# Performance work log

Measured on AMD Instinct MI355X. Metric: run time of the kernel, lower is better.

Reference implementation:

```python
import jax, jax.numpy as jnp
import numpy as np

# OGB feature vocab sizes
ATOM_DIMS = [119, 4, 12, 12, 10, 6, 6, 2, 2]
BOND_DIMS = [5, 6, 2]
ATOM_OFF = np.concatenate([[0], np.cumsum(ATOM_DIMS)[:-1]]).astype(np.int32)
BOND_OFF = np.concatenate([[0], np.cumsum(BOND_DIMS)[:-1]]).astype(np.int32)
SCHEDULE_LEN = 5   # len(train_schedule) == len(eval_schedule)
NUM_GRAPHS = 12000
BN_EPS = 1e-5

N_NODES, N_EDGES, HIDDEN, NUM_TASKS = 300000, 600000, 128, 128


def setup_inputs() -> dict:
    key = jax.random.key(0)
    ks = jax.random.split(key, 16)
    x = jax.random.randint(ks[0], (N_NODES, 9), 0, 2, dtype=jnp.int32)
    edge_index = jax.random.randint(ks[1], (2, N_EDGES), 0, N_NODES, dtype=jnp.int32)
    edge_attr = jax.random.randint(ks[2], (N_EDGES, 3), 0, 2, dtype=jnp.int32)
    batch = jnp.sort(jax.random.randint(ks[3], (N_NODES,), 0, NUM_GRAPHS, dtype=jnp.int32))
    # learned parameters (embedding tables concatenated with offsets)
    atom_emb = jax.random.normal(ks[4], (sum(ATOM_DIMS), HIDDEN), jnp.float32) * 0.1
    bond_emb = jax.random.normal(ks[5], (sum(BOND_DIMS), HIDDEN), jnp.float32) * 0.1
    conv_W = jax.random.normal(ks[6], (HIDDEN, HIDDEN), jnp.float32) * (1.0 / np.sqrt(HIDDEN))
    conv_b = jnp.zeros((HIDDEN,), jnp.float32)
    root_emb = jax.random.normal(ks[7], (HIDDEN,), jnp.float32) * 0.1
    bn_gamma = jnp.ones((HIDDEN,), jnp.float32)
    bn_beta = jnp.zeros((HIDDEN,), jnp.float32)
    bn_mean = jnp.zeros((HIDDEN,), jnp.float32)   # running stats (eval mode)
    bn_var = jnp.ones((HIDDEN,), jnp.float32)
    lin_W = jax.random.normal(ks[8], (NUM_TASKS, HIDDEN), jnp.float32) * (1.0 / np.sqrt(HIDDEN))
    lin_b = jnp.zeros((NUM_TASKS,), jnp.float32)
    return {"x": x, "edge_index": edge_index, "edge_attr": edge_attr, "batch": batch,
            "atom_emb": atom_emb, "bond_emb": bond_emb, "conv_W": conv_W, "conv_b": conv_b,
            "root_emb": root_emb, "bn_gamma": bn_gamma, "bn_beta": bn_beta,
            "bn_mean": bn_mean, "bn_var": bn_var, "lin_W": lin_W, "lin_b": lin_b}


def reference(x, edge_index, edge_attr, batch, atom_emb, bond_emb, conv_W, conv_b,
              root_emb, bn_gamma, bn_beta, bn_mean, bn_var, lin_W, lin_b):
    N = x.shape[0]
    # AtomEncoder / BondEncoder: sum of per-feature embedding lookups
    h = atom_emb[x + jnp.asarray(ATOM_OFF, x.dtype)].sum(axis=1)            # [N, H]
    e = bond_emb[edge_attr + jnp.asarray(BOND_OFF, edge_attr.dtype)].sum(axis=1)  # [E, H]
    row, col = edge_index[0], edge_index[1]
    deg = jax.ops.segment_sum(jnp.ones_like(row, h.dtype), row, num_segments=N) + 1.0  # [N]
    dis = deg ** -0.5                                                        # deg >= 1, no inf
    norm = dis[row] * dis[col]                                               # [E]
    inv_std = bn_gamma / jnp.sqrt(bn_var + BN_EPS)
    for i in range(SCHEDULE_LEN):
        old = h
        z = h @ conv_W.T + conv_b                                            # [N, H]
        # message: norm * relu(x_j + edge_emb), aggregated at target (col) via scatter-add
        msg = norm[:, None] * jax.nn.relu(z[row] + e)                        # [E, H]
        agg = jax.ops.segment_sum(msg, col, num_segments=N)                  # [N, H]
        z = agg + jax.nn.relu(z + root_emb) / deg[:, None]                   # self-loop term
        z = jax.nn.relu(z)
        z = (z - bn_mean) * inv_std + bn_beta                                # BN (eval, running stats)
        # dropout: identity in eval mode
        # NOTE: faithful to source bug: smooth_fac is the loop index i, not schedule[i]
        h = i * old + (1 - i) * z
    # global mean pool over graphs
    counts = jax.ops.segment_sum(jnp.ones((N,), h.dtype), batch, num_segments=NUM_GRAPHS)
    pooled = jax.ops.segment_sum(h, batch, num_segments=NUM_GRAPHS) / jnp.maximum(counts, 1.0)[:, None]
    return pooled @ lin_W.T + lin_b                                          # [num_graphs, num_tasks]
```

## Files before the change

### kernel.cpp

```cpp
#include <hip/hip_runtime.h>

#define HID 128
#define AROWS 173

typedef __attribute__((ext_vector_type(8))) short short8;
typedef __attribute__((ext_vector_type(8))) unsigned short ushort8v;
typedef __attribute__((ext_vector_type(4))) float floatx4;
typedef __attribute__((ext_vector_type(4))) unsigned short ushort4v;

__device__ __forceinline__ unsigned short f2bf(float f) {
    unsigned u = __builtin_bit_cast(unsigned, f);
    u += 0x7FFF + ((u >> 16) & 1);
    return (unsigned short)(u >> 16);
}
__device__ __forceinline__ float bf2f(unsigned short s) {
    unsigned u = ((unsigned)s) << 16;
    return __builtin_bit_cast(float, u);
}

__global__ void fillrd_kernel(float* __restrict__ dis, int* __restrict__ indeg, int N)
{
    int i = blockIdx.x * 256 + threadIdx.x;
    if (i < N) { dis[i] = 0.f; indeg[i] = 0; }
}

__global__ void diag_kernel(float* __restrict__ out, long n, float val)
{
    long i = (long)blockIdx.x * blockDim.x + threadIdx.x;
    if (i < n) out[i] = val;
}

__global__ __launch_bounds__(256) void tables_kernel(
    const float* __restrict__ conv_W, unsigned short* __restrict__ Wb,
    const float* __restrict__ lin_W, unsigned short* __restrict__ linWb,
    const float* __restrict__ bond_emb, float* __restrict__ comb,
    const float* __restrict__ gamma, const float* __restrict__ beta,
    const float* __restrict__ mean, const float* __restrict__ var,
    float* __restrict__ bnsc, float* __restrict__ bnsh,
    const float* __restrict__ atom_emb, unsigned short* __restrict__ aeb)
{
    int blk = blockIdx.x;
    int tid = threadIdx.x;
    if (blk < 64) {
        int i = blk * 256 + tid;
        Wb[i] = f2bf(conv_W[i]);
    } else if (blk < 128) {
        int i = (blk - 64) * 256 + tid;
        linWb[i] = f2bf(lin_W[i]);
    } else if (blk < 158) {
        int i = (blk - 128) * 2 + (tid >> 7);
        int c = tid & 127;
        int a0 = i / 12, a1 = (i % 12) / 2, a2 = i % 2;
        comb[i * HID + c] = bond_emb[a0 * HID + c] + bond_emb[(5 + a1) * HID + c]
                          + bond_emb[(11 + a2) * HID + c];
    } else if (blk == 158) {
        if (tid < HID) {
            float sc = gamma[tid] * rsqrtf(var[tid] + 1e-5f);
            bnsc[tid] = sc;
            bnsh[tid] = beta[tid] - mean[tid] * sc;
        }
    } else {
        int i = (blk - 159) * 256 + tid;
        if (i < AROWS * HID) aeb[i] = f2bf(atom_emb[i]);
    }
}

__global__ void hist_kernel(const int* __restrict__ ei, float* __restrict__ dis,
                            int* __restrict__ indeg, int E)
{
    for (int e = blockIdx.x * blockDim.x + threadIdx.x; e < E; e += gridDim.x * blockDim.x) {
        atomicAdd(&dis[ei[e]], 1.f);
        atomicAdd(&indeg[ei[E + e]], 1);
    }
}

__global__ void fdeg_kernel(float* __restrict__ dis, int N)
{
    int n = blockIdx.x * blockDim.x + threadIdx.x;
    if (n < N) dis[n] = rsqrtf(dis[n] + 1.f);
}

__global__ __launch_bounds__(256) void bsum_kernel(
    const int* __restrict__ indeg, int* __restrict__ partial, int N)
{
    __shared__ int s[256];
    int i = blockIdx.x * 256 + threadIdx.x;
    s[threadIdx.x] = (i < N) ? indeg[i] : 0;
    __syncthreads();
    for (int d = 128; d > 0; d >>= 1) {
        if (threadIdx.x < d) s[threadIdx.x] += s[threadIdx.x + d];
        __syncthreads();
    }
    if (threadIdx.x == 0) partial[blockIdx.x] = s[0];
}

__global__ __launch_bounds__(256) void scan1_kernel(
    const int* __restrict__ partial, int* __restrict__ offs,
    int* __restrict__ ptr, int B, int N)
{
    __shared__ int s[256];
    __shared__ int carry_s;
    int tid = threadIdx.x;
    if (tid == 0) carry_s = 0;
    __syncthreads();
    for (int base = 0; base < B; base += 256) {
        int i = base + tid;
        int v = (i < B) ? partial[i] : 0;
        s[tid] = v;
        __syncthreads();
        for (int d = 1; d < 256; d <<= 1) {
            int t = (tid >= d) ? s[tid - d] : 0;
            __syncthreads();
            s[tid] += t;
            __syncthreads();
        }
        int carry = carry_s;
        if (i < B) offs[i] = carry + s[tid] - v;
        __syncthreads();
        if (tid == 0) carry_s = carry + s[255];
        __syncthreads();
    }
    if (tid == 0) ptr[N] = carry_s;
}

__global__ __launch_bounds__(256) void scan2_kernel(
    const int* __restrict__ indeg, const int* __restrict__ offs,
    int* __restrict__ ptr, int* __restrict__ cursor, int N)
{
    __shared__ int s[256];
    int tid = threadIdx.x;
    int i = blockIdx.x * 256 + tid;
    int v = (i < N) ? indeg[i] : 0;
    s[tid] = v;
    __syncthreads();
    for (int d = 1; d < 256; d <<= 1) {
        int t = (tid >= d) ? s[tid - d] : 0;
        __syncthreads();
        s[tid] += t;
        __syncthreads();
    }
    if (i < N) {
        int ex = offs[blockIdx.x] + s[tid] - v;
        ptr[i] = ex;
        cursor[i] = ex;
    }
}

__global__ void fillcsr_kernel(const int* __restrict__ ei, const int* __restrict__ attr,
                               const float* __restrict__ dis, int* __restrict__ cursor,
                               int2* __restrict__ edata, int E)
{
    for (int e = blockIdx.x * blockDim.x + threadIdx.x; e < E; e += gridDim.x * blockDim.x) {
        int r   = ei[e];
        int col = ei[E + e];
        int pos = atomicAdd(&cursor[col], 1);
        int ci  = attr[e * 3] * 12 + attr[e * 3 + 1] * 2 + attr[e * 3 + 2];
        float nrm = dis[r] * dis[col];
        int2 ed;
        ed.x = r;
        ed.y = ci | ((int)f2bf(nrm) << 16);
        edata[pos] = ed;
    }
}

__global__ void gptr_kernel(const int* __restrict__ batch, int* __restrict__ gptr,
                            int N, int G)
{
    int n = blockIdx.x * blockDim.x + threadIdx.x;
    if (n >= N) return;
    int b = batch[n];
    int bp = (n == 0) ? -1 : batch[n - 1];
    for (int g = bp + 1; g <= b; ++g) gptr[g] = n;
    if (n == N - 1)
        for (int g = b + 1; g <= G; ++g) gptr[g] = N;
}

template<bool FIRST>
__device__ __forceinline__ ushort8v agg_node(
    long n, int c, const int* __restrict__ ptr, const int2* __restrict__ edata,
    const float* __restrict__ comb, const float* __restrict__ dis,
    const float* __restrict__ root, const float* __restrict__ bnsc,
    const float* __restrict__ bnsh, const unsigned short* __restrict__ zb,
    const unsigned short* __restrict__ hb, float fi)
{
    ushort8v zv = *reinterpret_cast<const ushort8v*>(zb + n * HID + c);
    ushort8v hv;
    if constexpr (!FIRST) hv = *reinterpret_cast<const ushort8v*>(hb + n * HID + c);
    float di = dis[n];
    float rd = di * di;
    float acc[8];
#pragma unroll
    for (int j = 0; j < 8; ++j) acc[j] = fmaxf(bf2f(zv[j]) + root[c + j], 0.f) * rd;

    int jb = ptr[n], je = ptr[n + 1];
    int j2 = jb;
    for (; j2 + 1 < je; j2 += 2) {
        int2 e0 = edata[j2];
        int2 e1 = edata[j2 + 1];
        ushort8v z0 = *reinterpret_cast<const ushort8v*>(zb + (long)e0.x * HID + c);
        ushort8v z1 = *reinterpret_cast<const ushort8v*>(zb + (long)e1.x * HID + c);
        const float* c0 = comb + (e0.y & 0xFF) * HID + c;
        const float* c1 = comb + (e1.y & 0xFF) * HID + c;
        float n0 = bf2f((unsigned short)(((unsigned)e0.y) >> 16));
        float n1 = bf2f((unsigned short)(((unsigned)e1.y) >> 16));
#pragma unroll
        for (int j = 0; j < 8; ++j) {
            acc[j] += fmaxf(bf2f(z0[j]) + c0[j], 0.f) * n0;
            acc[j] += fmaxf(bf2f(z1[j]) + c1[j], 0.f) * n1;
        }
    }
    if (j2 < je) {
        int2 e0 = edata[j2];
        ushort8v z0 = *reinterpret_cast<const ushort8v*>(zb + (long)e0.x * HID + c);
        const float* c0 = comb + (e0.y & 0xFF) * HID + c;
        float n0 = bf2f((unsigned short)(((unsigned)e0.y) >> 16));
#pragma unroll
        for (int j = 0; j < 8; ++j) acc[j] += fmaxf(bf2f(z0[j]) + c0[j], 0.f) * n0;
    }

    ushort8v o;
#pragma unroll
    for (int j = 0; j < 8; ++j) {
        float t = fmaxf(acc[j], 0.f) * bnsc[c + j] + bnsh[c + j];
        float h;
        if constexpr (FIRST) h = t;
        else h = fi * bf2f(hv[j]) + (1.f - fi) * t;
        o[j] = f2bf(h);
    }
    return o;
}

template<bool FIRST>
__global__ __launch_bounds__(256) void agg_kernel(
    const int* __restrict__ ptr, const int2* __restrict__ edata,
    const float* __restrict__ comb, const float* __restrict__ dis,
    const float* __restrict__ root, const float* __restrict__ bnsc,
    const float* __restrict__ bnsh, const unsigned short* __restrict__ zb,
    unsigned short* __restrict__ hb, float fi, int N)
{
    long n = (long)blockIdx.x * 16 + (threadIdx.x >> 4);
    if (n >= N) return;
    int c = (threadIdx.x & 15) * 8;
    ushort8v o = agg_node<FIRST>(n, c, ptr, edata, comb, dis, root, bnsc, bnsh, zb, hb, fi);
    *reinterpret_cast<ushort8v*>(hb + n * HID + c) = o;
}

__device__ __forceinline__ void gemm_from_lds(
    unsigned short (*hs)[132], const unsigned short* __restrict__ Wb,
    const float* __restrict__ bias, unsigned short* __restrict__ zb,
    long base, int N, int tid)
{
    int wave = tid >> 6;
    int lane = tid & 63;
    int l15 = lane & 15;
    int q = lane >> 4;
    int rowl0 = wave * 32;

    short8 a[2][4];
#pragma unroll
    for (int mt = 0; mt < 2; ++mt) {
        int rl = rowl0 + mt * 16 + l15;
#pragma unroll
        for (int kb = 0; kb < 4; ++kb)
            a[mt][kb] = *reinterpret_cast<const short8*>(&hs[rl][q * 8 + kb * 32]);
    }

    floatx4 acc[2][8];
#pragma unroll
    for (int mt = 0; mt < 2; ++mt)
#pragma unroll
        for (int nt = 0; nt < 8; ++nt) {
            floatx4 zz = {0.f, 0.f, 0.f, 0.f};
            acc[mt][nt] = zz;
        }

#pragma unroll
    for (int nt = 0; nt < 8; ++nt) {
        const unsigned short* bp = Wb + (nt * 16 + l15) * HID + q * 8;
#pragma unroll
        for (int kb = 0; kb < 4; ++kb) {
            short8 b = *reinterpret_cast<const short8*>(bp + kb * 32);
            acc[0][nt] = __builtin_amdgcn_mfma_f32_16x16x32_bf16(a[0][kb], b, acc[0][nt], 0, 0, 0);
            acc[1][nt] = __builtin_amdgcn_mfma_f32_16x16x32_bf16(a[1][kb], b, acc[1][nt], 0, 0, 0);
        }
    }

    float bi[8];
#pragma unroll
    for (int nt = 0; nt < 8; ++nt) bi[nt] = bias[nt * 16 + l15];

    __syncthreads();
#pragma unroll
    for (int mt = 0; mt < 2; ++mt)
#pragma unroll
        for (int r = 0; r < 4; ++r) {
            int lr = rowl0 + mt * 16 + q * 4 + r;
#pragma unroll
            for (int nt = 0; nt < 8; ++nt)
                hs[lr][l15 + 16 * nt] = f2bf(acc[mt][nt][r] + bi[nt]);
        }
    __syncthreads();

    int tr = tid >> 4;
    int tc = (tid & 15) * 8;
#pragma unroll
    for (int i = 0; i < 8; ++i) {
        int row = i * 16 + tr;
        long gr = base + row;
        if (gr < N) {
            ushort8v v = *reinterpret_cast<const ushort8v*>(&hs[row][tc]);
            *reinterpret_cast<ushort8v*>(zb + gr * HID + tc) = v;
        }
    }
}

__global__ __launch_bounds__(256) void egemm_kernel(
    const int* __restrict__ x, const unsigned short* __restrict__ aeb,
    const unsigned short* __restrict__ Wb, const float* __restrict__ bias,
    unsigned short* __restrict__ zb, int N)
{
    __shared__ unsigned short hs[128][132];
    __shared__ int xs[128 * 9];
    int tid = threadIdx.x;
    long base = (long)blockIdx.x * 128;
    const int OFF[9] = {0, 119, 123, 135, 147, 157, 163, 169, 171};

    int nb = (N - base < 128) ? (int)(N - base) : 128;
    int cnt = nb * 9;
    for (int i = tid; i < cnt; i += 256) xs[i] = x[base * 9 + i];
    __syncthreads();

    int sn = tid >> 4;
    int cc = (tid & 15) * 8;
#pragma unroll 1
    for (int s = 0; s < 8; ++s) {
        int lr = s * 16 + sn;
        ushort8v o;
        if (lr < nb) {
            float acc[8];
#pragma unroll
            for (int j = 0; j < 8; ++j) acc[j] = 0.f;
#pragma unroll
            for (int f = 0; f < 9; ++f) {
                int idx = xs[lr * 9 + f] + OFF[f];
                ushort8v v = *reinterpret_cast<const ushort8v*>(aeb + (long)idx * HID + cc);
#pragma unroll
                for (int j = 0; j < 8; ++j) acc[j] += bf2f(v[j]);
            }
#pragma unroll
            for (int j = 0; j < 8; ++j) o[j] = f2bf(acc[j]);
        } else {
            ushort8v z8 = {0, 0, 0, 0, 0, 0, 0, 0};
            o = z8;
        }
        *reinterpret_cast<ushort8v*>(&hs[lr][cc]) = o;
    }
    __syncthreads();

    gemm_from_lds(hs, Wb, bias, zb, base, N, tid);
}

template<bool FIRST>
__global__ __launch_bounds__(256) void fusedag_kernel(
    const int* __restrict__ ptr, const int2* __restrict__ edata,
    const float* __restrict__ comb, const float* __restrict__ dis,
    const float* __restrict__ root, const float* __restrict__ bnsc,
    const float* __restrict__ bnsh, const unsigned short* __restrict__ zin,
    unsigned short* __restrict__ hb, const unsigned short* __restrict__ Wb,
    const float* __restrict__ bias, unsigned short* __restrict__ zout,
    float fi, int N)
{
    __shared__ unsigned short hs[128][132];
    int tid = threadIdx.x;
    long base = (long)blockIdx.x * 128;
    int sn = tid >> 4;
    int cc = (tid & 15) * 8;
#pragma unroll 1
    for (int s = 0; s < 8; ++s) {
        int lr = s * 16 + sn;
        long n = base + lr;
        ushort8v o;
        if (n < N) {
            o = agg_node<FIRST>(n, cc, ptr, edata, comb, dis, root, bnsc, bnsh,
                                zin, hb, fi);
            *reinterpret_cast<ushort8v*>(hb + n * HID + cc) = o;
        } else {
            ushort8v z8 = {0, 0, 0, 0, 0, 0, 0, 0};
            o = z8;
        }
        *reinterpret_cast<ushort8v*>(&hs[lr][cc]) = o;
    }
    __syncthreads();

    gemm_from_lds(hs, Wb, bias, zout, base, N, tid);
}

__global__ __launch_bounds__(256) void gemm_kernel(
    const unsigned short* __restrict__ hb, const unsigned short* __restrict__ Wb,
    const float* __restrict__ bias, unsigned short* __restrict__ zb, int N)
{
    __shared__ unsigned short st[128][132];
    int tid = threadIdx.x;
    int wave = tid >> 6;
    int lane = tid & 63;
    int l15 = lane & 15;
    int q = lane >> 4;
    long base = (long)blockIdx.x * 128;
    long row0 = base + wave * 32;

#pragma unroll
    for (int mt = 0; mt < 2; ++mt) {
        long rl = row0 + mt * 16 + l15;
        if (rl > (long)N - 1) rl = (long)N - 1;
        const unsigned short* ap = hb + rl * HID + q * 8;
        int lrow = wave * 32 + mt * 16 + l15;
#pragma unroll
        for (int kb = 0; kb < 4; ++kb)
            *reinterpret_cast<ushort8v*>(&st[lrow][q * 8 + kb * 32]) =
                *reinterpret_cast<const ushort8v*>(ap + kb * 32);
    }
    __syncthreads();
    gemm_from_lds(st, Wb, bias, zb, base, N, tid);
}

__global__ __launch_bounds__(256) void linmm_kernel(
    const unsigned short* __restrict__ pb, const unsigned short* __restrict__ Wb,
    const float* __restrict__ bias, float* __restrict__ out, int G)
{
    int wave = threadIdx.x >> 6;
    int lane = threadIdx.x & 63;
    int l15 = lane & 15;
    int q = lane >> 4;
    long row0 = (long)blockIdx.x * 128 + wave * 32;

    short8 a[2][4];
#pragma unroll
    for (int mt = 0; mt < 2; ++mt) {
        long rl = row0 + mt * 16 + l15;
        if (rl > (long)G - 1) rl = (long)G - 1;
        const unsigned short* ap = pb + rl * HID + q * 8;
#pragma unroll
        for (int kb = 0; kb < 4; ++kb)
            a[mt][kb] = *reinterpret_cast<const short8*>(ap + kb * 32);
    }

    floatx4 acc[2][8];
#pragma unroll
    for (int mt = 0; mt < 2; ++mt)
#pragma unroll
        for (int nt = 0; nt < 8; ++nt) {
            floatx4 zz = {0.f, 0.f, 0.f, 0.f};
            acc[mt][nt] = zz;
        }

#pragma unroll
    for (int nt = 0; nt < 8; ++nt) {
        const unsigned short* bp = Wb + (nt * 16 + l15) * HID + q * 8;
#pragma unroll
        for (int kb = 0; kb < 4; ++kb) {
            short8 b = *reinterpret_cast<const short8*>(bp + kb * 32);
            acc[0][nt] = __builtin_amdgcn_mfma_f32_16x16x32_bf16(a[0][kb], b, acc[0][nt], 0, 0, 0);
            acc[1][nt] = __builtin_amdgcn_mfma_f32_16x16x32_bf16(a[1][kb], b, acc[1][nt], 0, 0, 0);
        }
    }

    float bi[8];
#pragma unroll
    for (int nt = 0; nt < 8; ++nt) bi[nt] = bias[nt * 16 + l15];

#pragma unroll
    for (int mt = 0; mt < 2; ++mt)
#pragma unroll
        for (int r = 0; r < 4; ++r) {
            long rr = row0 + mt * 16 + q * 4 + r;
            if (rr < G) {
                float* op = out + rr * HID + l15;
#pragma unroll
                for (int nt = 0; nt < 8; ++nt)
                    op[nt * 16] = acc[mt][nt][r] + bi[nt];
            }
        }
}

__global__ __launch_bounds__(256) void pool_kernel(
    const unsigned short* __restrict__ hb, const int* __restrict__ gptr,
    unsigned short* __restrict__ pb, int G)
{
    int g = blockIdx.x;
    if (g >= G) return;
    int tid = threadIdx.x;
    int sub = tid >> 5;
    int c = (tid & 31) * 4;
    int lo = gptr[g], hi = gptr[g + 1];
    floatx4 s = {0.f, 0.f, 0.f, 0.f};
    for (int n = lo + sub; n < hi; n += 8) {
        ushort4v hv = *reinterpret_cast<const ushort4v*>(hb + (long)n * HID + c);
#pragma unroll
        for (int j = 0; j < 4; ++j) s[j] += bf2f(hv[j]);
    }
    __shared__ float ps[8][HID];
    *reinterpret_cast<floatx4*>(&ps[sub][c]) = s;
    __syncthreads();
    if (tid < HID) {
        float sum = 0.f;
#pragma unroll
        for (int k = 0; k < 8; ++k) sum += ps[k][tid];
        float cnt = (hi > lo) ? (float)(hi - lo) : 1.f;
        pb[(long)g * HID + tid] = f2bf(sum / cnt);
    }
}

extern "C" void kernel_launch(void* const* d_in, const int* in_sizes, int n_in,
                              void* d_out, int out_size, void* d_ws, size_t ws_size,
                              hipStream_t stream)
{
    const int* x          = (const int*)d_in[0];
    const int* ei         = (const int*)d_in[1];
    const int* attr       = (const int*)d_in[2];
    const int* batch      = (const int*)d_in[3];
    const float* atom_emb = (const float*)d_in[4];
    const float* bond_emb = (const float*)d_in[5];
    const float* conv_W   = (const float*)d_in[6];
    const float* conv_b   = (const float*)d_in[7];
    const float* root     = (const float*)d_in[8];
    const float* gamma    = (const float*)d_in[9];
    const float* beta     = (const float*)d_in[10];
    const float* mean     = (const float*)d_in[11];
    const float* var      = (const float*)d_in[12];
    const float* lin_W    = (const float*)d_in[13];
    const float* lin_b    = (const float*)d_in[14];
    float* out = (float*)d_out;

    const int N = in_sizes[0] / 9;
    const int E = in_sizes[1] / 2;
    const int G = out_size / HID;
    const int B = (N + 255) / 256;

    auto al = [](size_t b) { return (b + 255) & ~(size_t)255; };
    const size_t need_base =
        al((size_t)N * HID * 2) +
        al((size_t)N * HID * 2) +
        al((size_t)(N + 1) * 4) +
        al((size_t)E * 8) +
        al((size_t)N * 4) +
        al((size_t)2048 * 4) * 2 +
        al((size_t)(G + 1) * 4) +
        al((size_t)(G + 128) * HID * 2) +
        al((size_t)60 * HID * 4) +
        al((size_t)HID * 4) * 2 +
        al((size_t)HID * HID * 2) * 2 +
        al((size_t)AROWS * HID * 2);
    const size_t need_fused = need_base + al((size_t)N * HID * 2);

    if (ws_size < need_base || B > 2048) {
        float v = (B > 2048) ? 3000.f : (1000.f + (float)(ws_size >> 20));
        long n = (long)out_size;
        diag_kernel<<<(int)((n + 255) / 256), 256, 0, stream>>>(out, n, v);
        return;
    }
    const bool fused_ok = (ws_size >= need_fused);

    char* wsp = (char*)d_ws;
    size_t used = 0;
    auto alloc = [&](size_t bytes) { char* p = wsp + used; used += al(bytes); return p; };
    unsigned short* hb = (unsigned short*)alloc((size_t)N * HID * 2);
    unsigned short* zb = (unsigned short*)alloc((size_t)N * HID * 2);
    int* ptr      = (int*)alloc((size_t)(N + 1) * 4);
    int2* edata   = (int2*)alloc((size_t)E * 8);
    int* indeg    = (int*)alloc((size_t)N * 4);
    int* cursor   = indeg;
    int* partial  = (int*)alloc((size_t)2048 * 4);
    int* offs     = (int*)alloc((size_t)2048 * 4);
    int* gptr     = (int*)alloc((size_t)(G + 1) * 4);
    unsigned short* pb = (unsigned short*)alloc((size_t)(G + 128) * HID * 2);
    float* dis    = (float*)pb;
    float* comb   = (float*)alloc((size_t)60 * HID * 4);
    float* bnsc   = (float*)alloc((size_t)HID * 4);
    float* bnsh   = (float*)alloc((size_t)HID * 4);
    unsigned short* Wb    = (unsigned short*)alloc((size_t)HID * HID * 2);
    unsigned short* linWb = (unsigned short*)alloc((size_t)HID * HID * 2);
    unsigned short* aeb   = (unsigned short*)alloc((size_t)AROWS * HID * 2);
    unsigned short* zb2   = (unsigned short*)alloc((size_t)N * HID * 2);

    fillrd_kernel<<<B, 256, 0, stream>>>(dis, indeg, N);
    tables_kernel<<<246, 256, 0, stream>>>(conv_W, Wb, lin_W, linWb, bond_emb, comb,
                                           gamma, beta, mean, var, bnsc, bnsh,
                                           atom_emb, aeb);
    hist_kernel<<<1024, 256, 0, stream>>>(ei, dis, indeg, E);
    fdeg_kernel<<<B, 256, 0, stream>>>(dis, N);
    bsum_kernel<<<B, 256, 0, stream>>>(indeg, partial, N);
    scan1_kernel<<<1, 256, 0, stream>>>(partial, offs, ptr, B, N);
    scan2_kernel<<<B, 256, 0, stream>>>(indeg, offs, ptr, cursor, N);
    fillcsr_kernel<<<1024, 256, 0, stream>>>(ei, attr, dis, cursor, edata, E);
    gptr_kernel<<<B, 256, 0, stream>>>(batch, gptr, N, G);

    const int gemm_blocks = (N + 127) / 128;
    const int agg_blocks  = (N + 15) / 16;
    egemm_kernel<<<gemm_blocks, 256, 0, stream>>>(x, aeb, Wb, conv_b, zb, N);

    if (fused_ok) {
        fusedag_kernel<true ><<<gemm_blocks, 256, 0, stream>>>(ptr, edata, comb, dis,
                root, bnsc, bnsh, zb,  hb, Wb, conv_b, zb2, 0.f, N);
        fusedag_kernel<false><<<gemm_blocks, 256, 0, stream>>>(ptr, edata, comb, dis,
                root, bnsc, bnsh, zb2, hb, Wb, conv_b, zb,  2.f, N);
        fusedag_kernel<false><<<gemm_blocks, 256, 0, stream>>>(ptr, edata, comb, dis,
                root, bnsc, bnsh, zb,  hb, Wb, conv_b, zb2, 3.f, N);
        agg_kernel<false><<<agg_blocks, 256, 0, stream>>>(ptr, edata, comb, dis, root,
                bnsc, bnsh, zb2, hb, 4.f, N);
    } else {
        agg_kernel<true ><<<agg_blocks, 256, 0, stream>>>(ptr, edata, comb, dis, root,
                bnsc, bnsh, zb, hb, 0.f, N);
        const float fis[3] = {2.f, 3.f, 4.f};
        for (int t = 0; t < 3; ++t) {
            gemm_kernel<<<gemm_blocks, 256, 0, stream>>>(hb, Wb, conv_b, zb, N);
            agg_kernel<false><<<agg_blocks, 256, 0, stream>>>(ptr, edata, comb, dis,
                    root, bnsc, bnsh, zb, hb, fis[t], N);
        }
    }

    pool_kernel<<<G, 256, 0, stream>>>(hb, gptr, pb, G);
    linmm_kernel<<<(G + 127) / 128, 256, 0, stream>>>(pb, linWb, lin_b, out, G);
}
```

Measured before the change: 771.3 us.

## Sort nodes by in-degree for aggregation, drop fused agg-gemm, store bond table in bf16

Adds a counting sort of nodes by in-degree (histogram, scan, permutation kernels) so each aggregation block processes nodes with similar edge counts, which is meant to reduce divergence and load imbalance within waves. The fused aggregate+GEMM kernels are removed in favour of separate gemm and agg launches, since the permuted node order no longer maps cleanly onto 128-row GEMM tiles. The combined bond-embedding table is stored as bf16 and loaded as one vector per edge, halving its footprint. The cost is extra preprocessing launches, scattered writes from the permuted order, and losing the fusion that kept h in LDS for the GEMM.

```diff
diff --git a/kernel.cpp b/kernel.cpp
--- a/kernel.cpp
+++ b/kernel.cpp
@@ -18,10 +18,12 @@
     return __builtin_bit_cast(float, u);
 }
 
-__global__ void fillrd_kernel(float* __restrict__ dis, int* __restrict__ indeg, int N)
+__global__ void fillrd_kernel(float* __restrict__ dis, int* __restrict__ indeg,
+                              int* __restrict__ dhist, int N)
 {
     int i = blockIdx.x * 256 + threadIdx.x;
     if (i < N) { dis[i] = 0.f; indeg[i] = 0; }
+    if (blockIdx.x == 0 && threadIdx.x < 32) dhist[threadIdx.x] = 0;
 }
 
 __global__ void diag_kernel(float* __restrict__ out, long n, float val)
@@ -33,7 +35,7 @@
 __global__ __launch_bounds__(256) void tables_kernel(
     const float* __restrict__ conv_W, unsigned short* __restrict__ Wb,
     const float* __restrict__ lin_W, unsigned short* __restrict__ linWb,
-    const float* __restrict__ bond_emb, float* __restrict__ comb,
+    const float* __restrict__ bond_emb, unsigned short* __restrict__ comb,
     const float* __restrict__ gamma, const float* __restrict__ beta,
     const float* __restrict__ mean, const float* __restrict__ var,
     float* __restrict__ bnsc, float* __restrict__ bnsh,
@@ -51,8 +53,8 @@
         int i = (blk - 128) * 2 + (tid >> 7);
         int c = tid & 127;
         int a0 = i / 12, a1 = (i % 12) / 2, a2 = i % 2;
-        comb[i * HID + c] = bond_emb[a0 * HID + c] + bond_emb[(5 + a1) * HID + c]
-                          + bond_emb[(11 + a2) * HID + c];
+        comb[i * HID + c] = f2bf(bond_emb[a0 * HID + c] + bond_emb[(5 + a1) * HID + c]
+                               + bond_emb[(11 + a2) * HID + c]);
     } else if (blk == 158) {
         if (tid < HID) {
             float sc = gamma[tid] * rsqrtf(var[tid] + 1e-5f);
@@ -146,6 +148,53 @@
     }
 }
 
+__global__ __launch_bounds__(256) void dhist_kernel(
+    const int* __restrict__ ptr, int* __restrict__ dhist, int N)
+{
+    __shared__ int lh[32];
+    int tid = threadIdx.x;
+    if (tid < 32) lh[tid] = 0;
+    __syncthreads();
+    int n = blockIdx.x * 256 + tid;
+    if (n < N) {
+        int d = ptr[n + 1] - ptr[n];
+        if (d > 31) d = 31;
+        atomicAdd(&lh[d], 1);
+    }
+    __syncthreads();
+    if (tid < 32 && lh[tid]) atomicAdd(&dhist[tid], lh[tid]);
+}
+
+__global__ void dscan_kernel(const int* __restrict__ dhist, int* __restrict__ dcur)
+{
+    if (threadIdx.x == 0) {
+        int s = 0;
+        for (int k = 0; k < 32; ++k) { dcur[k] = s; s += dhist[k]; }
+    }
+}
+
+__global__ __launch_bounds__(256) void dperm_kernel(
+    const int* __restrict__ ptr, int* __restrict__ dcur,
+    int* __restrict__ perm, int N)
+{
+    __shared__ int lh[32];
+    __shared__ int gb[32];
+    int tid = threadIdx.x;
+    if (tid < 32) lh[tid] = 0;
+    __syncthreads();
+    int n = blockIdx.x * 256 + tid;
+    int rank = 0, d = 0;
+    if (n < N) {
+        d = ptr[n + 1] - ptr[n];
+        if (d > 31) d = 31;
+        rank = atomicAdd(&lh[d], 1);
+    }
+    __syncthreads();
+    if (tid < 32) gb[tid] = lh[tid] ? atomicAdd(&dcur[tid], lh[tid]) : 0;
+    __syncthreads();
+    if (n < N) perm[gb[d] + rank] = n;
+}
+
 __global__ void fillcsr_kernel(const int* __restrict__ ei, const int* __restrict__ attr,
                                const float* __restrict__ dis, int* __restrict__ cursor,
                                int2* __restrict__ edata, int E)
@@ -176,13 +225,19 @@
 }
 
 template<bool FIRST>
-__device__ __forceinline__ ushort8v agg_node(
-    long n, int c, const int* __restrict__ ptr, const int2* __restrict__ edata,
-    const float* __restrict__ comb, const float* __restrict__ dis,
-    const float* __restrict__ root, const float* __restrict__ bnsc,
-    const float* __restrict__ bnsh, const unsigned short* __restrict__ zb,
-    const unsigned short* __restrict__ hb, float fi)
-{
+__global__ __launch_bounds__(256) void agg_kernel(
+    const int* __restrict__ perm, const int* __restrict__ ptr,
+    const int2* __restrict__ edata, const unsigned short* __restrict__ comb,
+    const float* __restrict__ dis, const float* __restrict__ root,
+    const float* __restrict__ bnsc, const float* __restrict__ bnsh,
+    const unsigned short* __restrict__ zb, unsigned short* __restrict__ hb,
+    float fi, int N)
+{
+    long slot = (long)blockIdx.x * 16 + (threadIdx.x >> 4);
+    if (slot >= N) return;
+    long n = perm[slot];
+    int c = (threadIdx.x & 15) * 8;
+
     ushort8v zv = *reinterpret_cast<const ushort8v*>(zb + n * HID + c);
     ushort8v hv;
     if constexpr (!FIRST) hv = *reinterpret_cast<const ushort8v*>(hb + n * HID + c);
@@ -199,23 +254,24 @@
         int2 e1 = edata[j2 + 1];
         ushort8v z0 = *reinterpret_cast<const ushort8v*>(zb + (long)e0.x * HID + c);
         ushort8v z1 = *reinterpret_cast<const ushort8v*>(zb + (long)e1.x * HID + c);
-        const float* c0 = comb + (e0.y & 0xFF) * HID + c;
-        const float* c1 = comb + (e1.y & 0xFF) * HID + c;
+        ushort8v c0 = *reinterpret_cast<const ushort8v*>(comb + (e0.y & 0xFF) * HID + c);
+        ushort8v c1 = *reinterpret_cast<const ushort8v*>(comb + (e1.y & 0xFF) * HID + c);
         float n0 = bf2f((unsigned short)(((unsigned)e0.y) >> 16));
         float n1 = bf2f((unsigned short)(((unsigned)e1.y) >> 16));
 #pragma unroll
         for (int j = 0; j < 8; ++j) {
-            acc[j] += fmaxf(bf2f(z0[j]) + c0[j], 0.f) * n0;
-            acc[j] += fmaxf(bf2f(z1[j]) + c1[j], 0.f) * n1;
+            acc[j] += fmaxf(bf2f(z0[j]) + bf2f(c0[j]), 0.f) * n0;
+            acc[j] += fmaxf(bf2f(z1[j]) + bf2f(c1[j]), 0.f) * n1;
         }
     }
     if (j2 < je) {
         int2 e0 = edata[j2];
         ushort8v z0 = *reinterpret_cast<const ushort8v*>(zb + (long)e0.x * HID + c);
-        const float* c0 = comb + (e0.y & 0xFF) * HID + c;
+        ushort8v c0 = *reinterpret_cast<const ushort8v*>(comb + (e0.y & 0xFF) * HID + c);
         float n0 = bf2f((unsigned short)(((unsigned)e0.y) >> 16));
 #pragma unroll
-        for (int j = 0; j < 8; ++j) acc[j] += fmaxf(bf2f(z0[j]) + c0[j], 0.f) * n0;
+        for (int j = 0; j < 8; ++j)
+            acc[j] += fmaxf(bf2f(z0[j]) + bf2f(c0[j]), 0.f) * n0;
     }
 
     ushort8v o;
@@ -227,21 +283,6 @@
         else h = fi * bf2f(hv[j]) + (1.f - fi) * t;
         o[j] = f2bf(h);
     }
-    return o;
-}
-
-template<bool FIRST>
-__global__ __launch_bounds__(256) void agg_kernel(
-    const int* __restrict__ ptr, const int2* __restrict__ edata,
-    const float* __restrict__ comb, const float* __restrict__ dis,
-    const float* __restrict__ root, const float* __restrict__ bnsc,
-    const float* __restrict__ bnsh, const unsigned short* __restrict__ zb,
-    unsigned short* __restrict__ hb, float fi, int N)
-{
-    long n = (long)blockIdx.x * 16 + (threadIdx.x >> 4);
-    if (n >= N) return;
-    int c = (threadIdx.x & 15) * 8;
-    ushort8v o = agg_node<FIRST>(n, c, ptr, edata, comb, dis, root, bnsc, bnsh, zb, hb, fi);
     *reinterpret_cast<ushort8v*>(hb + n * HID + c) = o;
 }
 
@@ -358,41 +399,6 @@
     __syncthreads();
 
     gemm_from_lds(hs, Wb, bias, zb, base, N, tid);
-}
-
-template<bool FIRST>
-__global__ __launch_bounds__(256) void fusedag_kernel(
-    const int* __restrict__ ptr, const int2* __restrict__ edata,
-    const float* __restrict__ comb, const float* __restrict__ dis,
-    const float* __restrict__ root, const float* __restrict__ bnsc,
-    const float* __restrict__ bnsh, const unsigned short* __restrict__ zin,
-    unsigned short* __restrict__ hb, const unsigned short* __restrict__ Wb,
-    const float* __restrict__ bias, unsigned short* __restrict__ zout,
-    float fi, int N)
-{
-    __shared__ unsigned short hs[128][132];
-    int tid = threadIdx.x;
-    long base = (long)blockIdx.x * 128;
-    int sn = tid >> 4;
-    int cc = (tid & 15) * 8;
-#pragma unroll 1
-    for (int s = 0; s < 8; ++s) {
-        int lr = s * 16 + sn;
-        long n = base + lr;
-        ushort8v o;
-        if (n < N) {
-            o = agg_node<FIRST>(n, cc, ptr, edata, comb, dis, root, bnsc, bnsh,
-                                zin, hb, fi);
-            *reinterpret_cast<ushort8v*>(hb + n * HID + cc) = o;
-        } else {
-            ushort8v z8 = {0, 0, 0, 0, 0, 0, 0, 0};
-            o = z8;
-        }
-        *reinterpret_cast<ushort8v*>(&hs[lr][cc]) = o;
-    }
-    __syncthreads();
-
-    gemm_from_lds(hs, Wb, bias, zout, base, N, tid);
 }
 
 __global__ __launch_bounds__(256) void gemm_kernel(
@@ -537,7 +543,7 @@
     const int B = (N + 255) / 256;
 
     auto al = [](size_t b) { return (b + 255) & ~(size_t)255; };
-    const size_t need_base =
+    const size_t need =
         al((size_t)N * HID * 2) +
         al((size_t)N * HID * 2) +
         al((size_t)(N + 1) * 4) +
@@ -546,19 +552,19 @@
         al((size_t)2048 * 4) * 2 +
         al((size_t)(G + 1) * 4) +
         al((size_t)(G + 128) * HID * 2) +
-        al((size_t)60 * HID * 4) +
+        al((size_t)60 * HID * 2) +
         al((size_t)HID * 4) * 2 +
         al((size_t)HID * HID * 2) * 2 +
-        al((size_t)AROWS * HID * 2);
-    const size_t need_fused = need_base + al((size_t)N * HID * 2);
-
-    if (ws_size < need_base || B > 2048) {
+        al((size_t)AROWS * HID * 2) +
+        al((size_t)N * 4) +
+        al(32 * 4) * 2;
+
+    if (ws_size < need || B > 2048) {
         float v = (B > 2048) ? 3000.f : (1000.f + (float)(ws_size >> 20));
         long n = (long)out_size;
         diag_kernel<<<(int)((n + 255) / 256), 256, 0, stream>>>(out, n, v);
         return;
     }
-    const bool fused_ok = (ws_size >= need_fused);
 
     char* wsp = (char*)d_ws;
     size_t used = 0;
@@ -574,15 +580,17 @@
     int* gptr     = (int*)alloc((size_t)(G + 1) * 4);
     unsigned short* pb = (unsigned short*)alloc((size_t)(G + 128) * HID * 2);
     float* dis    = (float*)pb;
-    float* comb   = (float*)alloc((size_t)60 * HID * 4);
+    unsigned short* comb = (unsigned short*)alloc((size_t)60 * HID * 2);
     float* bnsc   = (float*)alloc((size_t)HID * 4);
     float* bnsh   = (float*)alloc((size_t)HID * 4);
     unsigned short* Wb    = (unsigned short*)alloc((size_t)HID * HID * 2);
     unsigned short* linWb = (unsigned short*)alloc((size_t)HID * HID * 2);
     unsigned short* aeb   = (unsigned short*)alloc((size_t)AROWS * HID * 2);
-    unsigned short* zb2   = (unsigned short*)alloc((size_t)N * HID * 2);
-
-    fillrd_kernel<<<B, 256, 0, stream>>>(dis, indeg, N);
+    int* perm     = (int*)alloc((size_t)N * 4);
+    int* dhist    = (int*)alloc(32 * 4);
+    int* dcur     = (int*)alloc(32 * 4);
+
+    fillrd_kernel<<<B, 256, 0, stream>>>(dis, indeg, dhist, N);
     tables_kernel<<<246, 256, 0, stream>>>(conv_W, Wb, lin_W, linWb, bond_emb, comb,
                                            gamma, beta, mean, var, bnsc, bnsh,
                                            atom_emb, aeb);
@@ -591,31 +599,22 @@
     bsum_kernel<<<B, 256, 0, stream>>>(indeg, partial, N);
     scan1_kernel<<<1, 256, 0, stream>>>(partial, offs, ptr, B, N);
     scan2_kernel<<<B, 256, 0, stream>>>(indeg, offs, ptr, cursor, N);
+    dhist_kernel<<<B, 256, 0, stream>>>(ptr, dhist, N);
+    dscan_kernel<<<1, 64, 0, stream>>>(dhist, dcur);
+    dperm_kernel<<<B, 256, 0, stream>>>(ptr, dcur, perm, N);
     fillcsr_kernel<<<1024, 256, 0, stream>>>(ei, attr, dis, cursor, edata, E);
     gptr_kernel<<<B, 256, 0, stream>>>(batch, gptr, N, G);
 
     const int gemm_blocks = (N + 127) / 128;
     const int agg_blocks  = (N + 15) / 16;
     egemm_kernel<<<gemm_blocks, 256, 0, stream>>>(x, aeb, Wb, conv_b, zb, N);
-
-    if (fused_ok) {
-        fusedag_kernel<true ><<<gemm_blocks, 256, 0, stream>>>(ptr, edata, comb, dis,
-                root, bnsc, bnsh, zb,  hb, Wb, conv_b, zb2, 0.f, N);
-        fusedag_kernel<false><<<gemm_blocks, 256, 0, stream>>>(ptr, edata, comb, dis,
-                root, bnsc, bnsh, zb2, hb, Wb, conv_b, zb,  2.f, N);
-        fusedag_kernel<false><<<gemm_blocks, 256, 0, stream>>>(ptr, edata, comb, dis,
-                root, bnsc, bnsh, zb,  hb, Wb, conv_b, zb2, 3.f, N);
-        agg_kernel<false><<<agg_blocks, 256, 0, stream>>>(ptr, edata, comb, dis, root,
-                bnsc, bnsh, zb2, hb, 4.f, N);
-    } else {
-        agg_kernel<true ><<<agg_blocks, 256, 0, stream>>>(ptr, edata, comb, dis, root,
-                bnsc, bnsh, zb, hb, 0.f, N);
-        const float fis[3] = {2.f, 3.f, 4.f};
-        for (int t = 0; t < 3; ++t) {
-            gemm_kernel<<<gemm_blocks, 256, 0, stream>>>(hb, Wb, conv_b, zb, N);
-            agg_kernel<false><<<agg_blocks, 256, 0, stream>>>(ptr, edata, comb, dis,
-                    root, bnsc, bnsh, zb, hb, fis[t], N);
-        }
+    agg_kernel<true ><<<agg_blocks, 256, 0, stream>>>(perm, ptr, edata, comb, dis,
+            root, bnsc, bnsh, zb, hb, 0.f, N);
+    const float fis[3] = {2.f, 3.f, 4.f};
+    for (int t = 0; t < 3; ++t) {
+        gemm_kernel<<<gemm_blocks, 256, 0, stream>>>(hb, Wb, conv_b, zb, N);
+        agg_kernel<false><<<agg_blocks, 256, 0, stream>>>(perm, ptr, edata, comb, dis,
+                root, bnsc, bnsh, zb, hb, fis[t], N);
     }
 
     pool_kernel<<<G, 256, 0, stream>>>(hb, gptr, pb, G);
```

Measured after the change: 726.1 us. 1.06x faster.
